# Kernel tuning notes

Measured on AMD Instinct MI355X. Metric: run time of the kernel, lower is better.

Reference implementation:

```python
import jax, jax.numpy as jnp
import numpy as np

B, S, D = 4, 2048, 1024
H = 16            # n_heads
HD = D // H       # head_dim = 64
F = 64            # feature_dim of linear-attention feature map


def setup_inputs() -> dict:
    key = jax.random.key(0)
    ks = jax.random.split(key, 16)
    w = lambda k, shape: jax.random.normal(k, shape, dtype=jnp.float32) * 0.02
    return {
        "x": jax.random.normal(ks[0], (B, S, D), dtype=jnp.float32),
        # flash-attention branch params (Linear stored as [in, out])
        "fq": w(ks[1], (D, D)),
        "fk": w(ks[2], (D, D)),
        "fv": w(ks[3], (D, D)),
        "fo_w": w(ks[4], (D, D)),
        "fo_b": jnp.zeros((D,), jnp.float32),
        # linear-attention branch params
        "lq": w(ks[5], (D, D)),
        "lk": w(ks[6], (D, D)),
        "lv": w(ks[7], (D, D)),
        "lo_w": w(ks[8], (D, D)),
        "lo_b": jnp.zeros((D,), jnp.float32),
        "fm_w": w(ks[9], (HD, F)),
        "fm_b": jnp.zeros((F,), jnp.float32),
        # gate
        "gate_w": w(ks[10], (D, 1)),
        "gate_b": jnp.zeros((1,), jnp.float32),
    }


def reference(x, fq, fk, fv, fo_w, fo_b, lq, lk, lv, lo_w, lo_b,
              fm_w, fm_b, gate_w, gate_b):
    b, s, d = x.shape
    # ---- flash (standard softmax) attention path ----
    q = (x @ fq).reshape(b, s, H, HD)
    k = (x @ fk).reshape(b, s, H, HD)
    v = (x @ fv).reshape(b, s, H, HD)
    scale = 1.0 / np.sqrt(HD).astype(np.float32)
    scores = jnp.einsum('bqhd,bkhd->bhqk', q, k) * scale
    attn = jax.nn.softmax(scores, axis=-1)
    flash = jnp.einsum('bhqk,bkhd->bqhd', attn, v).reshape(b, s, d)
    flash_out = flash @ fo_w + fo_b
    # ---- linear (kernelized) attention path ----
    ql = (x @ lq).reshape(b, s, H, HD)
    kl = (x @ lk).reshape(b, s, H, HD)
    vl = (x @ lv).reshape(b, s, H, HD)
    qf = jax.nn.relu(ql @ fm_w + fm_b)   # [b,s,h,f]
    kf = jax.nn.relu(kl @ fm_w + fm_b)
    kv = jnp.einsum('blhf,blhd->bhfd', kf, vl)
    lin = jnp.einsum('blhf,bhfd->blhd', qf, kv)
    k_sum = kf.sum(axis=1)                               # [b,h,f]
    norm = jnp.einsum('blhf,bhf->blh', qf, k_sum)[..., None]
    lin = lin / jnp.maximum(norm, 1e-6)
    linear_out = lin.reshape(b, s, d) @ lo_w + lo_b
    # ---- sigmoid gate blend ----
    gate = jax.nn.sigmoid(x @ gate_w + gate_b)           # [b,s,1]
    return gate * flash_out + (1.0 - gate) * linear_out
```

## Files before the change

### kernel.cpp

```cpp
#include <hip/hip_runtime.h>
#include <math.h>

typedef __attribute__((ext_vector_type(4))) float f32x4;
typedef __attribute__((ext_vector_type(16))) float f32x16;
typedef __attribute__((ext_vector_type(8))) short s16x8;
typedef __attribute__((ext_vector_type(8))) unsigned short u16x8;

constexpr int Bc = 4, Sc = 2048, Dc = 1024, Hc = 16, HDc = 64, Fc = 64;
constexpr int Rc = Bc * Sc;
constexpr size_t MAT = (size_t)Rc * Dc;
constexpr int KST = 88;
constexpr int NCH = 16;

__device__ __forceinline__ float bf2f(unsigned short u) {
    union { unsigned int i; float f; } v; v.i = ((unsigned int)u) << 16; return v.f;
}
__device__ __forceinline__ unsigned short f2bf(float f) {
    union { float f; unsigned int i; } v; v.f = f;
    unsigned int r = v.i + 0x7FFFu + ((v.i >> 16) & 1u);
    return (unsigned short)(r >> 16);
}
__device__ __forceinline__ unsigned cvtpk(float a, float b) {
    unsigned r;
    asm("v_cvt_pk_bf16_f32 %0, %1, %2" : "=v"(r) : "v"(a), "v"(b));
    return r;
}
__device__ __forceinline__ void async16(const void* g, void* l) {
    __builtin_amdgcn_global_load_lds(
        (const __attribute__((address_space(1))) unsigned int*)g,
        (__attribute__((address_space(3))) unsigned int*)l, 16, 0, 0);
}

__global__ __launch_bounds__(256) void gate_cvt(const float* __restrict__ x,
        const float* __restrict__ gw, const float* __restrict__ gb,
        float* __restrict__ G, unsigned short* __restrict__ Y) {
    const int lane = threadIdx.x & 63;
    const int wave = threadIdx.x >> 6;
    const int r = blockIdx.x * 4 + wave;
    const size_t base = (size_t)r * Dc;
    float acc = 0.f;
    #pragma unroll
    for (int i = 0; i < 4; ++i) {
        int off = (lane + 64 * i) * 4;
        float4 v = *(const float4*)(x + base + off);
        float4 w = *(const float4*)(gw + off);
        acc += v.x * w.x + v.y * w.y + v.z * w.z + v.w * w.w;
        ushort4 o;
        o.x = f2bf(v.x); o.y = f2bf(v.y); o.z = f2bf(v.z); o.w = f2bf(v.w);
        *(ushort4*)(Y + base + off) = o;
    }
    #pragma unroll
    for (int off = 32; off > 0; off >>= 1) acc += __shfl_down(acc, off, 64);
    if (lane == 0) {
        float z = acc + gb[0];
        G[r] = 1.f / (1.f + __expf(-z));
    }
}

__global__ __launch_bounds__(256) void wtrans(
        const float* W0, const float* W1, const float* W2, const float* W3,
        const float* W4, const float* W5, const float* W6, const float* W7,
        unsigned short* T0, unsigned short* T1, unsigned short* T2, unsigned short* T3,
        unsigned short* T4, unsigned short* T5, unsigned short* T6, unsigned short* T7) {
    const float* W; unsigned short* T;
    switch (blockIdx.z) {
        case 0: W = W0; T = T0; break;  case 1: W = W1; T = T1; break;
        case 2: W = W2; T = T2; break;  case 3: W = W3; T = T3; break;
        case 4: W = W4; T = T4; break;  case 5: W = W5; T = T5; break;
        case 6: W = W6; T = T6; break;  default: W = W7; T = T7; break;
    }
    __shared__ float tile[64][65];
    const int t = threadIdx.x;
    const int r0 = blockIdx.x * 64, c0 = blockIdx.y * 64;
    #pragma unroll
    for (int i = 0; i < 4; ++i) {
        int row = (t >> 4) + 16 * i, col = (t & 15) * 4;
        float4 v = *(const float4*)(W + (size_t)(r0 + row) * 1024 + c0 + col);
        tile[row][col] = v.x; tile[row][col + 1] = v.y;
        tile[row][col + 2] = v.z; tile[row][col + 3] = v.w;
    }
    __syncthreads();
    #pragma unroll
    for (int i = 0; i < 4; ++i) {
        int orow = (t >> 4) + 16 * i, ocol = (t & 15) * 4;
        ushort4 o;
        o.x = f2bf(tile[ocol][orow]);     o.y = f2bf(tile[ocol + 1][orow]);
        o.z = f2bf(tile[ocol + 2][orow]); o.w = f2bf(tile[ocol + 3][orow]);
        *(ushort4*)(T + (size_t)(c0 + orow) * 1024 + r0 + ocol) = o;
    }
}

__global__ __launch_bounds__(256) void gemm3(const unsigned short* __restrict__ A,
        const unsigned short* __restrict__ WT, unsigned short* __restrict__ C0,
        unsigned short* __restrict__ C1, unsigned short* __restrict__ C2) {
    __shared__ unsigned short As[128 * 32];
    __shared__ unsigned short Bs[128 * 32];
    const int tid = threadIdx.x, wave = tid >> 6, lane = tid & 63;
    const int brow = blockIdx.x * 128;
    const int bcolg = blockIdx.y * 128;
    unsigned short* C = (blockIdx.y < 8) ? C0 : (blockIdx.y < 16 ? C1 : C2);
    const int bcol = bcolg & 1023;
    const int wm = wave >> 1, wn = wave & 1;
    const int lr = lane & 15, g8 = (lane >> 4) * 8;
    const int srow = 32 * wave + (lane >> 2);
    const int scol = (lane & 3) * 8;
    f32x4 acc[4][4];
    #pragma unroll
    for (int m = 0; m < 4; ++m)
        #pragma unroll
        for (int n = 0; n < 4; ++n) acc[m][n] = (f32x4){0.f, 0.f, 0.f, 0.f};
    for (int k0 = 0; k0 < 1024; k0 += 32) {
        __syncthreads();
        #pragma unroll
        for (int i = 0; i < 2; ++i) {
            async16(A  + (size_t)(brow  + srow + 16 * i) * 1024 + k0 + scol, &As[(32 * wave + 16 * i) * 32]);
            async16(WT + (size_t)(bcolg + srow + 16 * i) * 1024 + k0 + scol, &Bs[(32 * wave + 16 * i) * 32]);
        }
        __syncthreads();
        s16x8 af[4], bf[4];
        #pragma unroll
        for (int m = 0; m < 4; ++m) af[m] = *(const s16x8*)&As[(64 * wm + 16 * m + lr) * 32 + g8];
        #pragma unroll
        for (int n = 0; n < 4; ++n) bf[n] = *(const s16x8*)&Bs[(64 * wn + 16 * n + lr) * 32 + g8];
        #pragma unroll
        for (int m = 0; m < 4; ++m)
            #pragma unroll
            for (int n = 0; n < 4; ++n)
                acc[m][n] = __builtin_amdgcn_mfma_f32_16x16x32_bf16(af[m], bf[n], acc[m][n], 0, 0, 0);
    }
    const int rg = (lane >> 4) * 4;
    #pragma unroll
    for (int m = 0; m < 4; ++m)
        #pragma unroll
        for (int n = 0; n < 4; ++n)
            #pragma unroll
            for (int j = 0; j < 4; ++j)
                C[(size_t)(brow + 64 * wm + 16 * m + rg + j) * 1024 + bcol + 64 * wn + 16 * n + lr] =
                    f2bf(acc[m][n][j]);
}

__global__ __launch_bounds__(256) void final_gemm(const unsigned short* __restrict__ A1,
        const unsigned short* __restrict__ WT1, const unsigned short* __restrict__ A2,
        const unsigned short* __restrict__ WT2, const float* __restrict__ b1,
        const float* __restrict__ b2, const float* __restrict__ G, float* __restrict__ OUT) {
    __shared__ unsigned short As[128 * 32];
    __shared__ unsigned short Bs[128 * 32];
    const int tid = threadIdx.x, wave = tid >> 6, lane = tid & 63;
    const int brow = blockIdx.x * 128, bcol = blockIdx.y * 128;
    const int wm = wave >> 1, wn = wave & 1;
    const int lr = lane & 15, g8 = (lane >> 4) * 8;
    const int srow = 32 * wave + (lane >> 2);
    const int scol = (lane & 3) * 8;
    f32x4 acc[4][4];
    #pragma unroll
    for (int m = 0; m < 4; ++m)
        #pragma unroll
        for (int n = 0; n < 4; ++n) acc[m][n] = (f32x4){0.f, 0.f, 0.f, 0.f};
    for (int pass = 0; pass < 2; ++pass) {
        const unsigned short* A  = pass ? A2 : A1;
        const unsigned short* WT = pass ? WT2 : WT1;
        for (int k0 = 0; k0 < 1024; k0 += 32) {
            __syncthreads();
            #pragma unroll
            for (int i = 0; i < 2; ++i) {
                async16(A  + (size_t)(brow + srow + 16 * i) * 1024 + k0 + scol, &As[(32 * wave + 16 * i) * 32]);
                async16(WT + (size_t)(bcol + srow + 16 * i) * 1024 + k0 + scol, &Bs[(32 * wave + 16 * i) * 32]);
            }
            __syncthreads();
            s16x8 af[4], bf[4];
            #pragma unroll
            for (int m = 0; m < 4; ++m) af[m] = *(const s16x8*)&As[(64 * wm + 16 * m + lr) * 32 + g8];
            #pragma unroll
            for (int n = 0; n < 4; ++n) bf[n] = *(const s16x8*)&Bs[(64 * wn + 16 * n + lr) * 32 + g8];
            #pragma unroll
            for (int m = 0; m < 4; ++m)
                #pragma unroll
                for (int n = 0; n < 4; ++n)
                    acc[m][n] = __builtin_amdgcn_mfma_f32_16x16x32_bf16(af[m], bf[n], acc[m][n], 0, 0, 0);
        }
    }
    const int rg = (lane >> 4) * 4;
    #pragma unroll
    for (int m = 0; m < 4; ++m)
        #pragma unroll
        for (int j = 0; j < 4; ++j) {
            int row = brow + 64 * wm + 16 * m + rg + j;
            float g = G[row];
            #pragma unroll
            for (int n = 0; n < 4; ++n) {
                int col = bcol + 64 * wn + 16 * n + lr;
                OUT[(size_t)row * 1024 + col] = acc[m][n][j] + g * b1[col] + (1.f - g) * b2[col];
            }
        }
}

__global__ __launch_bounds__(512) void flash_mfma(const unsigned short* __restrict__ Qg,
        const unsigned short* __restrict__ Kg, const unsigned short* __restrict__ Vg,
        const float* __restrict__ G, unsigned short* __restrict__ FA) {
    __shared__ unsigned short Ks[2][64 * KST];
    __shared__ unsigned short Vt[2][64 * KST];
    const int tid = threadIdx.x, wave = tid >> 6, lane = tid & 63;
    const int b = blockIdx.x >> 4, h = blockIdx.x & 15, q0 = blockIdx.y * 256;
    const int lq = lane & 31, hi = lane >> 5;
    const float QSCALE = 0.125f * 1.44269504f;
    const size_t qrow = (size_t)b * Sc + q0 + wave * 32 + lq;
    const size_t qoff = qrow * Dc + h * HDc + 8 * hi;
    s16x8 aq[4];
    #pragma unroll
    for (int dc = 0; dc < 4; ++dc) {
        u16x8 raw = *(const u16x8*)(Qg + qoff + 16 * dc);
        #pragma unroll
        for (int j = 0; j < 8; ++j) aq[dc][j] = (short)f2bf(bf2f(raw[j]) * QSCALE);
    }
    const s16x8 ones = {0x3F80, 0x3F80, 0x3F80, 0x3F80, 0x3F80, 0x3F80, 0x3F80, 0x3F80};
    f32x16 oacc[2], lacc;
    #pragma unroll
    for (int t = 0; t < 2; ++t)
        #pragma unroll
        for (int r = 0; r < 16; ++r) oacc[t][r] = 0.f;
    #pragma unroll
    for (int r = 0; r < 16; ++r) lacc[r] = 0.f;
    const int srow = tid >> 3, sc8 = (tid & 7) * 8, va = tid & 7;
    const int p0 = (srow & 3) | (((srow >> 3) & 1) << 2) | (((srow >> 2) & 1) << 3) | (srow & 0x30);
    const int pg = p0 >> 3, pin = p0 & 7;
    const size_t kvoff = (size_t)h * HDc + sc8;
    {
        size_t gg = ((size_t)b * Sc + srow) * Dc + kvoff;
        u16x8 kreg = *(const u16x8*)(Kg + gg);
        u16x8 vreg = *(const u16x8*)(Vg + gg);
        *(u16x8*)&Ks[0][srow * KST + sc8] = kreg;
        #pragma unroll
        for (int j = 0; j < 8; ++j)
            Vt[0][(sc8 + j) * KST + 8 * (pg ^ va) + pin] = vreg[j];
    }
    __syncthreads();
    int cur = 0;
    for (int t0 = 0; t0 < Sc; t0 += 64) {
        const bool nxt = (t0 + 64) < Sc;
        u16x8 kn, vn;
        if (nxt) {
            size_t gg = ((size_t)b * Sc + t0 + 64 + srow) * Dc + kvoff;
            kn = *(const u16x8*)(Kg + gg);
            vn = *(const u16x8*)(Vg + gg);
        }
        f32x16 s2[2];
        #pragma unroll
        for (int t = 0; t < 2; ++t)
            #pragma unroll
            for (int r = 0; r < 16; ++r) s2[t][r] = 0.f;
        __builtin_amdgcn_s_setprio(1);
        #pragma unroll
        for (int kt2 = 0; kt2 < 2; ++kt2)
            #pragma unroll
            for (int dc = 0; dc < 4; ++dc) {
                s16x8 ak = *(const s16x8*)&Ks[cur][(32 * kt2 + lq) * KST + 16 * dc + 8 * hi];
                s2[kt2] = __builtin_amdgcn_mfma_f32_32x32x16_bf16(ak, aq[dc], s2[kt2], 0, 0, 0);
            }
        __builtin_amdgcn_s_setprio(0);
        #pragma unroll
        for (int t = 0; t < 2; ++t)
            #pragma unroll
            for (int r = 0; r < 16; ++r)
                s2[t][r] = exp2f(s2[t][r]);
        s16x8 pf[4];
        #pragma unroll
        for (int kc = 0; kc < 4; ++kc) {
            const int t = kc >> 1, e = 8 * (kc & 1);
            union { s16x8 v; unsigned u[4]; } w;
            w.u[0] = cvtpk(s2[t][e + 0], s2[t][e + 1]);
            w.u[1] = cvtpk(s2[t][e + 2], s2[t][e + 3]);
            w.u[2] = cvtpk(s2[t][e + 4], s2[t][e + 5]);
            w.u[3] = cvtpk(s2[t][e + 6], s2[t][e + 7]);
            pf[kc] = w.v;
        }
        __builtin_amdgcn_s_setprio(1);
        #pragma unroll
        for (int dtile = 0; dtile < 2; ++dtile) {
            const int row = 32 * dtile + lq;
            const int rsw = (row >> 3) & 7;
            #pragma unroll
            for (int kc = 0; kc < 4; ++kc) {
                const int g = 4 * (kc >> 1) + 2 * (kc & 1) + hi;
                s16x8 av = *(const s16x8*)&Vt[cur][row * KST + 8 * (g ^ rsw)];
                oacc[dtile] = __builtin_amdgcn_mfma_f32_32x32x16_bf16(av, pf[kc], oacc[dtile], 0, 0, 0);
            }
        }
        #pragma unroll
        for (int kc = 0; kc < 4; ++kc)
            lacc = __builtin_amdgcn_mfma_f32_32x32x16_bf16(ones, pf[kc], lacc, 0, 0, 0);
        __builtin_amdgcn_s_setprio(0);
        if (nxt) {
            *(u16x8*)&Ks[cur ^ 1][srow * KST + sc8] = kn;
            #pragma unroll
            for (int j = 0; j < 8; ++j)
                Vt[cur ^ 1][(sc8 + j) * KST + 8 * (pg ^ va) + pin] = vn[j];
        }
        __syncthreads();
        cur ^= 1;
    }
    const float scl = G[qrow] / lacc[0];
    #pragma unroll
    for (int dtile = 0; dtile < 2; ++dtile)
        #pragma unroll
        for (int s = 0; s < 4; ++s) {
            ushort4 o4;
            o4.x = f2bf(oacc[dtile][4 * s + 0] * scl);
            o4.y = f2bf(oacc[dtile][4 * s + 1] * scl);
            o4.z = f2bf(oacc[dtile][4 * s + 2] * scl);
            o4.w = f2bf(oacc[dtile][4 * s + 3] * scl);
            *(ushort4*)(FA + qrow * Dc + h * HDc + 32 * dtile + 8 * s + 4 * hi) = o4;
        }
}

__global__ __launch_bounds__(256) void featmap_kernel(unsigned short* __restrict__ QL,
        unsigned short* __restrict__ KL, const float* __restrict__ fmw, const float* __restrict__ fmb) {
    __shared__ float Wf[64][68];
    __shared__ float bs[64];
    __shared__ float Xs[16][68];
    const int tid = threadIdx.x;
    for (int i = tid; i < 64 * 64 / 4; i += 256) {
        int r = i >> 4, c = (i & 15) << 2;
        *(float4*)&Wf[r][c] = *(const float4*)(fmw + r * 64 + c);
    }
    if (tid < 64) bs[tid] = fmb[tid];
    const size_t row0 = (size_t)blockIdx.x * 16;
    const int rr = tid >> 4;
    const int fg = (tid & 15) << 2;
    for (int pass = 0; pass < 2; ++pass) {
        unsigned short* X = pass ? KL : QL;
        __syncthreads();
        {
            int r = tid >> 4, c = (tid & 15) << 2;
            ushort4 xv = *(const ushort4*)(X + (row0 + r) * 64 + c);
            Xs[r][c] = bf2f(xv.x); Xs[r][c + 1] = bf2f(xv.y);
            Xs[r][c + 2] = bf2f(xv.z); Xs[r][c + 3] = bf2f(xv.w);
        }
        __syncthreads();
        float a0 = bs[fg], a1 = bs[fg + 1], a2 = bs[fg + 2], a3 = bs[fg + 3];
        #pragma unroll 8
        for (int d = 0; d < 64; ++d) {
            float xv = Xs[rr][d];
            float4 w = *(const float4*)&Wf[d][fg];
            a0 += xv * w.x; a1 += xv * w.y; a2 += xv * w.z; a3 += xv * w.w;
        }
        ushort4 ov;
        ov.x = f2bf(fmaxf(a0, 0.f)); ov.y = f2bf(fmaxf(a1, 0.f));
        ov.z = f2bf(fmaxf(a2, 0.f)); ov.w = f2bf(fmaxf(a3, 0.f));
        *(ushort4*)(X + (row0 + rr) * 64 + fg) = ov;
    }
}

__global__ __launch_bounds__(256) void kv_part(const unsigned short* __restrict__ KF,
        const unsigned short* __restrict__ VL, float* __restrict__ PART, float* __restrict__ PARTS) {
    __shared__ float Ks[32][68];
    __shared__ float Vs[32][68];
    const int tid = threadIdx.x;
    const int bh = blockIdx.x;
    const int b = bh >> 4, h = bh & 15;
    const int ch = blockIdx.y;
    const int f = tid >> 2;
    const int dg = (tid & 3) << 4;
    float acc[16] = {};
    float ksum = 0.f;
    const int lbeg = ch * (Sc / NCH), lend = lbeg + Sc / NCH;
    for (int l0 = lbeg; l0 < lend; l0 += 32) {
        __syncthreads();
        for (int i = tid; i < 32 * 64 / 4; i += 256) {
            int r = i >> 4, c = (i & 15) << 2;
            size_t gg = ((size_t)(b * Sc + l0 + r) * Hc + h) * 64 + c;
            ushort4 kk = *(const ushort4*)(KF + gg);
            ushort4 vv = *(const ushort4*)(VL + gg);
            Ks[r][c] = bf2f(kk.x); Ks[r][c + 1] = bf2f(kk.y);
            Ks[r][c + 2] = bf2f(kk.z); Ks[r][c + 3] = bf2f(kk.w);
            Vs[r][c] = bf2f(vv.x); Vs[r][c + 1] = bf2f(vv.y);
            Vs[r][c + 2] = bf2f(vv.z); Vs[r][c + 3] = bf2f(vv.w);
        }
        __syncthreads();
        #pragma unroll 4
        for (int ll = 0; ll < 32; ++ll) {
            float kf = Ks[ll][f];
            ksum += kf;
            float4 v0 = *(const float4*)&Vs[ll][dg];
            float4 v1 = *(const float4*)&Vs[ll][dg + 4];
            float4 v2 = *(const float4*)&Vs[ll][dg + 8];
            float4 v3 = *(const float4*)&Vs[ll][dg + 12];
            acc[0] += kf * v0.x; acc[1] += kf * v0.y; acc[2]  += kf * v0.z; acc[3]  += kf * v0.w;
            acc[4] += kf * v1.x; acc[5] += kf * v1.y; acc[6]  += kf * v1.z; acc[7]  += kf * v1.w;
            acc[8] += kf * v2.x; acc[9] += kf * v2.y; acc[10] += kf * v2.z; acc[11] += kf * v2.w;
            acc[12] += kf * v3.x; acc[13] += kf * v3.y; acc[14] += kf * v3.z; acc[15] += kf * v3.w;
        }
    }
    size_t o = (((size_t)ch * 64 + bh) * 64 + f) * 64 + dg;
    *(float4*)(PART + o)      = make_float4(acc[0], acc[1], acc[2], acc[3]);
    *(float4*)(PART + o + 4)  = make_float4(acc[4], acc[5], acc[6], acc[7]);
    *(float4*)(PART + o + 8)  = make_float4(acc[8], acc[9], acc[10], acc[11]);
    *(float4*)(PART + o + 12) = make_float4(acc[12], acc[13], acc[14], acc[15]);
    if ((tid & 3) == 0) PARTS[((size_t)ch * 64 + bh) * 64 + f] = ksum;
}

__global__ __launch_bounds__(256) void kv_reduce(const float* __restrict__ PART,
        float* __restrict__ KV) {
    size_t i = (size_t)blockIdx.x * 256 + threadIdx.x;
    float s = 0.f;
    #pragma unroll
    for (int ch = 0; ch < NCH; ++ch) s += PART[(size_t)ch * 262144 + i];
    KV[i] = s;
}
__global__ __launch_bounds__(256) void ks_reduce(const float* __restrict__ PARTS,
        float* __restrict__ KS) {
    int i = blockIdx.x * 256 + threadIdx.x;
    float s = 0.f;
    #pragma unroll
    for (int ch = 0; ch < NCH; ++ch) s += PARTS[ch * 4096 + i];
    KS[i] = s;
}

__global__ __launch_bounds__(256) void kvb_build(const float* __restrict__ KV,
        const float* __restrict__ KS, unsigned short* __restrict__ KVB) {
    const int bh = blockIdx.x, t = threadIdx.x;
    for (int i = t; i < 80 * 64; i += 256) {
        int n = i >> 6, f = i & 63;
        float v = (n < 64) ? KV[(size_t)bh * 4096 + f * 64 + n]
                           : (n == 64 ? KS[bh * 64 + f] : 0.f);
        KVB[(size_t)bh * 5120 + i] = f2bf(v);
    }
}

__global__ __launch_bounds__(256) void lin_mfma(const unsigned short* __restrict__ QF,
        const unsigned short* __restrict__ KVB, const float* __restrict__ G,
        unsigned short* __restrict__ LA) {
    __shared__ unsigned short As[128 * 72];
    __shared__ unsigned short Bs[80 * 72];
    const int tid = threadIdx.x, wave = tid >> 6, lane = tid & 63;
    const int bh = blockIdx.y, b = bh >> 4, h = bh & 15;
    const size_t rowg0 = (size_t)b * Sc + blockIdx.x * 128;
    #pragma unroll
    for (int i = 0; i < 4; ++i) {
        int idx = tid + 256 * i;
        int r = idx >> 3, c8 = (idx & 7) * 8;
        *(u16x8*)&As[r * 72 + c8] = *(const u16x8*)(QF + (rowg0 + r) * 1024 + h * 64 + c8);
    }
    #pragma unroll
    for (int i = 0; i < 3; ++i) {
        int idx = tid + 256 * i;
        if (idx < 640) {
            int r = idx >> 3, c8 = (idx & 7) * 8;
            *(u16x8*)&Bs[r * 72 + c8] = *(const u16x8*)(KVB + (size_t)bh * 5120 + r * 64 + c8);
        }
    }
    __syncthreads();
    const int lr = lane & 15, g8 = (lane >> 4) * 8;
    f32x4 acc[2][5];
    #pragma unroll
    for (int m = 0; m < 2; ++m)
        #pragma unroll
        for (int n = 0; n < 5; ++n) acc[m][n] = (f32x4){0.f, 0.f, 0.f, 0.f};
    #pragma unroll
    for (int kc = 0; kc < 2; ++kc) {
        s16x8 af[2];
        #pragma unroll
        for (int m = 0; m < 2; ++m)
            af[m] = *(const s16x8*)&As[(32 * wave + 16 * m + lr) * 72 + kc * 32 + g8];
        #pragma unroll
        for (int n = 0; n < 5; ++n) {
            s16x8 bfv = *(const s16x8*)&Bs[(16 * n + lr) * 72 + kc * 32 + g8];
            #pragma unroll
            for (int m = 0; m < 2; ++m)
                acc[m][n] = __builtin_amdgcn_mfma_f32_16x16x32_bf16(af[m], bfv, acc[m][n], 0, 0, 0);
        }
    }
    const int rg = (lane >> 4) * 4;
    #pragma unroll
    for (int m = 0; m < 2; ++m)
        #pragma unroll
        for (int j = 0; j < 4; ++j) {
            size_t rglob = rowg0 + 32 * wave + 16 * m + rg + j;
            float g = G[rglob];
            float nv = __shfl(acc[m][4][j], lane & 48, 64);
            float inv = (1.f - g) / fmaxf(nv, 1e-6f);
            #pragma unroll
            for (int n = 0; n < 4; ++n)
                LA[rglob * 1024 + h * 64 + 16 * n + lr] = f2bf(acc[m][n][j] * inv);
        }
}

extern "C" void kernel_launch(void* const* d_in, const int* in_sizes, int n_in,
                              void* d_out, int out_size, void* d_ws, size_t ws_size,
                              hipStream_t stream) {
    const float* x   = (const float*)d_in[0];
    const float* fq  = (const float*)d_in[1];
    const float* fk  = (const float*)d_in[2];
    const float* fv  = (const float*)d_in[3];
    const float* fow = (const float*)d_in[4];
    const float* fob = (const float*)d_in[5];
    const float* lq  = (const float*)d_in[6];
    const float* lk  = (const float*)d_in[7];
    const float* lv  = (const float*)d_in[8];
    const float* low = (const float*)d_in[9];
    const float* lob = (const float*)d_in[10];
    const float* fmw = (const float*)d_in[11];
    const float* fmb = (const float*)d_in[12];
    const float* gw  = (const float*)d_in[13];
    const float* gb  = (const float*)d_in[14];
    float* out = (float*)d_out;

    char* p = (char*)d_ws;
    unsigned short* xb = (unsigned short*)p;          p += MAT * 2;
    unsigned short* wt_fq = (unsigned short*)p;       p += (size_t)1024 * 1024 * 2;
    unsigned short* wt_fk = (unsigned short*)p;       p += (size_t)1024 * 1024 * 2;
    unsigned short* wt_fv = (unsigned short*)p;       p += (size_t)1024 * 1024 * 2;
    unsigned short* wt_fo = (unsigned short*)p;       p += (size_t)1024 * 1024 * 2;
    unsigned short* wt_lq = (unsigned short*)p;       p += (size_t)1024 * 1024 * 2;
    unsigned short* wt_lk = (unsigned short*)p;       p += (size_t)1024 * 1024 * 2;
    unsigned short* wt_lv = (unsigned short*)p;       p += (size_t)1024 * 1024 * 2;
    unsigned short* wt_lo = (unsigned short*)p;       p += (size_t)1024 * 1024 * 2;
    unsigned short* P0 = (unsigned short*)p;          p += MAT * 2;
    unsigned short* P1 = (unsigned short*)p;          p += MAT * 2;
    unsigned short* P2 = (unsigned short*)p;          p += MAT * 2;
    unsigned short* FA = (unsigned short*)p;          p += MAT * 2;
    unsigned short* LA = (unsigned short*)p;          p += MAT * 2;
    float* KV = (float*)p;                            p += (size_t)Bc * Hc * Fc * HDc * 4;
    float* KS = (float*)p;                            p += (size_t)Bc * Hc * Fc * 4;
    float* G  = (float*)p;                            p += (size_t)Rc * 4;
    float* PART  = (float*)p;                         p += (size_t)NCH * 64 * 64 * 64 * 4;
    float* PARTS = (float*)p;                         p += (size_t)NCH * 64 * 64 * 4;
    unsigned short* KVB = (unsigned short*)p;         p += (size_t)64 * 80 * 64 * 2;

    dim3 proj3Grid(Rc / 128, 24);
    dim3 gemmGrid(Rc / 128, Dc / 128);

    gate_cvt<<<Rc / 4, 256, 0, stream>>>(x, gw, gb, G, xb);
    wtrans<<<dim3(16, 16, 8), 256, 0, stream>>>(fq, fk, fv, fow, lq, lk, lv, low,
            wt_fq, wt_fk, wt_fv, wt_fo, wt_lq, wt_lk, wt_lv, wt_lo);

    gemm3<<<proj3Grid, 256, 0, stream>>>(xb, wt_lq, P0, P1, P2);
    featmap_kernel<<<Rc * Hc / 16, 256, 0, stream>>>(P0, P1, fmw, fmb);
    kv_part<<<dim3(Bc * Hc, NCH), 256, 0, stream>>>(P1, P2, PART, PARTS);
    kv_reduce<<<(64 * 64 * 64) / 256, 256, 0, stream>>>(PART, KV);
    ks_reduce<<<(64 * 64) / 256, 256, 0, stream>>>(PARTS, KS);
    kvb_build<<<64, 256, 0, stream>>>(KV, KS, KVB);
    lin_mfma<<<dim3(Sc / 128, 64), 256, 0, stream>>>(P0, KVB, G, LA);

    gemm3<<<proj3Grid, 256, 0, stream>>>(xb, wt_fq, P0, P1, P2);
    flash_mfma<<<dim3(64, 8), 512, 0, stream>>>(P0, P1, P2, G, FA);

    final_gemm<<<gemmGrid, 256, 0, stream>>>(FA, wt_fo, LA, wt_lo, fob, lob, G, out);
}
```

Baseline: 386.1 us.

## Fold feature-map weights into Q/K projections and swizzle GEMM tiles per XCD

Precomputes combined weights W2 = Wq_head · fm_w (and the same for K), so the linear-branch projection GEMM writes relu(x·W2 + b) directly. This removes the separate featmap kernel and its extra read/write of the Q and K projections. It also remaps block indices in gemm3 and final_gemm so that blocks placed on the same XCD share row tiles, aiming for better L2 reuse. The cost is a small weight-build kernel each call, plus an extra bf16 rounding of the fused weights that may shift numerics slightly.

```diff
diff --git a/kernel.cpp b/kernel.cpp
--- a/kernel.cpp
+++ b/kernel.cpp
@@ -90,16 +90,62 @@
     }
 }
 
+__global__ __launch_bounds__(256) void w2build(const unsigned short* __restrict__ WTq,
+        const unsigned short* __restrict__ WTk, const float* __restrict__ fmw,
+        unsigned short* __restrict__ W2q, unsigned short* __restrict__ W2k) {
+    const int h = blockIdx.x, kc = blockIdx.y, mat = blockIdx.z;
+    const unsigned short* WTin = mat ? WTk : WTq;
+    unsigned short* W2out = mat ? W2k : W2q;
+    __shared__ float Wf[64][65];
+    __shared__ float Ws[64][129];
+    const int tid = threadIdx.x;
+    #pragma unroll
+    for (int i = 0; i < 4; ++i) {
+        int idx = tid + 256 * i;
+        int d = idx >> 4, c4 = (idx & 15) * 4;
+        float4 v = *(const float4*)(fmw + d * 64 + c4);
+        Wf[d][c4] = v.x; Wf[d][c4 + 1] = v.y; Wf[d][c4 + 2] = v.z; Wf[d][c4 + 3] = v.w;
+    }
+    #pragma unroll
+    for (int i = 0; i < 4; ++i) {
+        int idx = tid + 256 * i;
+        int d = idx >> 4, c8 = (idx & 15) * 8;
+        u16x8 v = *(const u16x8*)(WTin + (size_t)(h * 64 + d) * 1024 + kc * 128 + c8);
+        #pragma unroll
+        for (int j = 0; j < 8; ++j) Ws[d][c8 + j] = bf2f(v[j]);
+    }
+    __syncthreads();
+    const int f = tid & 63, kw = tid >> 6;
+    float acc[32];
+    #pragma unroll
+    for (int i = 0; i < 32; ++i) acc[i] = 0.f;
+    for (int d = 0; d < 64; ++d) {
+        float wf = Wf[d][f];
+        #pragma unroll
+        for (int i = 0; i < 32; ++i) acc[i] += wf * Ws[d][kw + 4 * i];
+    }
+    unsigned short* orow = W2out + (size_t)(h * 64 + f) * 1024 + kc * 128;
+    #pragma unroll
+    for (int i = 0; i < 32; ++i) orow[kw + 4 * i] = f2bf(acc[i]);
+}
+
 __global__ __launch_bounds__(256) void gemm3(const unsigned short* __restrict__ A,
-        const unsigned short* __restrict__ WT, unsigned short* __restrict__ C0,
-        unsigned short* __restrict__ C1, unsigned short* __restrict__ C2) {
+        const unsigned short* __restrict__ WTa, const unsigned short* __restrict__ WTb,
+        unsigned short* __restrict__ C0, unsigned short* __restrict__ C1,
+        unsigned short* __restrict__ C2, const float* __restrict__ fmb) {
     __shared__ unsigned short As[128 * 32];
     __shared__ unsigned short Bs[128 * 32];
     const int tid = threadIdx.x, wave = tid >> 6, lane = tid & 63;
-    const int brow = blockIdx.x * 128;
-    const int bcolg = blockIdx.y * 128;
-    unsigned short* C = (blockIdx.y < 8) ? C0 : (blockIdx.y < 16 ? C1 : C2);
-    const int bcol = bcolg & 1023;
+    const int lid = blockIdx.x + 64 * blockIdx.y;
+    const int xcd = lid & 7, seq = lid >> 3;
+    const int rp = 8 * xcd + (seq & 7);
+    const int cp = seq >> 3;
+    const int brow = rp * 128;
+    unsigned short* C = (cp < 8) ? C0 : (cp < 16 ? C1 : C2);
+    const int bcol = (cp & 7) * 128;
+    const unsigned short* WT = (cp < 16) ? (WTa + (size_t)cp * 128 * 1024)
+                                         : (WTb + (size_t)(cp - 16) * 128 * 1024);
+    const bool doRelu = (fmb != nullptr) && (cp < 16);
     const int wm = wave >> 1, wn = wave & 1;
     const int lr = lane & 15, g8 = (lane >> 4) * 8;
     const int srow = 32 * wave + (lane >> 2);
@@ -113,8 +159,8 @@
         __syncthreads();
         #pragma unroll
         for (int i = 0; i < 2; ++i) {
-            async16(A  + (size_t)(brow  + srow + 16 * i) * 1024 + k0 + scol, &As[(32 * wave + 16 * i) * 32]);
-            async16(WT + (size_t)(bcolg + srow + 16 * i) * 1024 + k0 + scol, &Bs[(32 * wave + 16 * i) * 32]);
+            async16(A  + (size_t)(brow + srow + 16 * i) * 1024 + k0 + scol, &As[(32 * wave + 16 * i) * 32]);
+            async16(WT + (size_t)(srow + 16 * i) * 1024 + k0 + scol, &Bs[(32 * wave + 16 * i) * 32]);
         }
         __syncthreads();
         s16x8 af[4], bf[4];
@@ -132,11 +178,16 @@
     #pragma unroll
     for (int m = 0; m < 4; ++m)
         #pragma unroll
-        for (int n = 0; n < 4; ++n)
-            #pragma unroll
-            for (int j = 0; j < 4; ++j)
+        for (int n = 0; n < 4; ++n) {
+            float bias = doRelu ? fmb[16 * n + lr] : 0.f;
+            #pragma unroll
+            for (int j = 0; j < 4; ++j) {
+                float v = acc[m][n][j];
+                if (doRelu) v = fmaxf(v + bias, 0.f);
                 C[(size_t)(brow + 64 * wm + 16 * m + rg + j) * 1024 + bcol + 64 * wn + 16 * n + lr] =
-                    f2bf(acc[m][n][j]);
+                    f2bf(v);
+            }
+        }
 }
 
 __global__ __launch_bounds__(256) void final_gemm(const unsigned short* __restrict__ A1,
@@ -146,7 +197,10 @@
     __shared__ unsigned short As[128 * 32];
     __shared__ unsigned short Bs[128 * 32];
     const int tid = threadIdx.x, wave = tid >> 6, lane = tid & 63;
-    const int brow = blockIdx.x * 128, bcol = blockIdx.y * 128;
+    const int lid = blockIdx.x + 64 * blockIdx.y;
+    const int xcd = lid & 7, seq = lid >> 3;
+    const int brow = (8 * xcd + (seq & 7)) * 128;
+    const int bcol = (seq >> 3) * 128;
     const int wm = wave >> 1, wn = wave & 1;
     const int lr = lane & 15, g8 = (lane >> 4) * 8;
     const int srow = 32 * wave + (lane >> 2);
@@ -310,44 +364,6 @@
             o4.w = f2bf(oacc[dtile][4 * s + 3] * scl);
             *(ushort4*)(FA + qrow * Dc + h * HDc + 32 * dtile + 8 * s + 4 * hi) = o4;
         }
-}
-
-__global__ __launch_bounds__(256) void featmap_kernel(unsigned short* __restrict__ QL,
-        unsigned short* __restrict__ KL, const float* __restrict__ fmw, const float* __restrict__ fmb) {
-    __shared__ float Wf[64][68];
-    __shared__ float bs[64];
-    __shared__ float Xs[16][68];
-    const int tid = threadIdx.x;
-    for (int i = tid; i < 64 * 64 / 4; i += 256) {
-        int r = i >> 4, c = (i & 15) << 2;
-        *(float4*)&Wf[r][c] = *(const float4*)(fmw + r * 64 + c);
-    }
-    if (tid < 64) bs[tid] = fmb[tid];
-    const size_t row0 = (size_t)blockIdx.x * 16;
-    const int rr = tid >> 4;
-    const int fg = (tid & 15) << 2;
-    for (int pass = 0; pass < 2; ++pass) {
-        unsigned short* X = pass ? KL : QL;
-        __syncthreads();
-        {
-            int r = tid >> 4, c = (tid & 15) << 2;
-            ushort4 xv = *(const ushort4*)(X + (row0 + r) * 64 + c);
-            Xs[r][c] = bf2f(xv.x); Xs[r][c + 1] = bf2f(xv.y);
-            Xs[r][c + 2] = bf2f(xv.z); Xs[r][c + 3] = bf2f(xv.w);
-        }
-        __syncthreads();
-        float a0 = bs[fg], a1 = bs[fg + 1], a2 = bs[fg + 2], a3 = bs[fg + 3];
-        #pragma unroll 8
-        for (int d = 0; d < 64; ++d) {
-            float xv = Xs[rr][d];
-            float4 w = *(const float4*)&Wf[d][fg];
-            a0 += xv * w.x; a1 += xv * w.y; a2 += xv * w.z; a3 += xv * w.w;
-        }
-        ushort4 ov;
-        ov.x = f2bf(fmaxf(a0, 0.f)); ov.y = f2bf(fmaxf(a1, 0.f));
-        ov.z = f2bf(fmaxf(a2, 0.f)); ov.w = f2bf(fmaxf(a3, 0.f));
-        *(ushort4*)(X + (row0 + rr) * 64 + fg) = ov;
-    }
 }
 
 __global__ __launch_bounds__(256) void kv_part(const unsigned short* __restrict__ KF,
@@ -525,6 +541,7 @@
     float* PART  = (float*)p;                         p += (size_t)NCH * 64 * 64 * 64 * 4;
     float* PARTS = (float*)p;                         p += (size_t)NCH * 64 * 64 * 4;
     unsigned short* KVB = (unsigned short*)p;         p += (size_t)64 * 80 * 64 * 2;
+    unsigned short* W2  = (unsigned short*)p;         p += (size_t)2 * 1024 * 1024 * 2;
 
     dim3 proj3Grid(Rc / 128, 24);
     dim3 gemmGrid(Rc / 128, Dc / 128);
@@ -532,16 +549,16 @@
     gate_cvt<<<Rc / 4, 256, 0, stream>>>(x, gw, gb, G, xb);
     wtrans<<<dim3(16, 16, 8), 256, 0, stream>>>(fq, fk, fv, fow, lq, lk, lv, low,
             wt_fq, wt_fk, wt_fv, wt_fo, wt_lq, wt_lk, wt_lv, wt_lo);
-
-    gemm3<<<proj3Grid, 256, 0, stream>>>(xb, wt_lq, P0, P1, P2);
-    featmap_kernel<<<Rc * Hc / 16, 256, 0, stream>>>(P0, P1, fmw, fmb);
+    w2build<<<dim3(16, 8, 2), 256, 0, stream>>>(wt_lq, wt_lk, fmw, W2, W2 + (size_t)1024 * 1024);
+
+    gemm3<<<proj3Grid, 256, 0, stream>>>(xb, W2, wt_lv, P0, P1, P2, fmb);
     kv_part<<<dim3(Bc * Hc, NCH), 256, 0, stream>>>(P1, P2, PART, PARTS);
     kv_reduce<<<(64 * 64 * 64) / 256, 256, 0, stream>>>(PART, KV);
     ks_reduce<<<(64 * 64) / 256, 256, 0, stream>>>(PARTS, KS);
     kvb_build<<<64, 256, 0, stream>>>(KV, KS, KVB);
     lin_mfma<<<dim3(Sc / 128, 64), 256, 0, stream>>>(P0, KVB, G, LA);
 
-    gemm3<<<proj3Grid, 256, 0, stream>>>(xb, wt_fq, P0, P1, P2);
+    gemm3<<<proj3Grid, 256, 0, stream>>>(xb, wt_fq, wt_fv, P0, P1, P2, nullptr);
     flash_mfma<<<dim3(64, 8), 512, 0, stream>>>(P0, P1, P2, G, FA);
 
     final_gemm<<<gemmGrid, 256, 0, stream>>>(FA, wt_fo, LA, wt_lo, fob, lob, G, out);
```

New measurement: 367.8 us. -4.7%, faster.
